# Kernel optimization log

Measured on AMD Instinct MI355X. Metric: run time of the kernel, lower is better.

## Reference

```python
import jax, jax.numpy as jnp
import numpy as np

INPUT_DIM = 2048
N_TREES = 15
TREE_DEPTH = 3
N_LEAVES = 2 ** TREE_DEPTH          # 8
N_INTERNAL = 2 ** TREE_DEPTH - 1    # 7
PARAM_PER_TREE = N_INTERNAL * (INPUT_DIM + 1) + N_LEAVES * 2  # 14375
BATCH = 32768


def setup_inputs() -> dict:
    key = jax.random.key(0)
    k1, k2, k3 = jax.random.split(key, 3)
    x = jax.random.normal(k1, (BATCH, INPUT_DIM), dtype=jnp.float32)
    tree_params = jax.random.normal(k2, (1, N_TREES * PARAM_PER_TREE), dtype=jnp.float32)
    tree_weights = jax.random.uniform(k3, (1, N_TREES), dtype=jnp.float32)
    return {"x": x, "tree_params": tree_params, "tree_weights": tree_weights}


def reference(x, tree_params, tree_weights):
    D, T, I, L = INPUT_DIM, N_TREES, N_INTERNAL, N_LEAVES
    B = x.shape[0]
    p = tree_params[0].reshape(T, PARAM_PER_TREE)
    split_w = p[:, : I * D].reshape(T, I, D)                       # [T, I, D]
    split_b = p[:, I * D : I * (D + 1)]                            # [T, I]
    leaf_logits = p[:, I * (D + 1) :].reshape(T, L, 2)             # [T, L, 2]

    # One fused GEMM over all trees/nodes: [B, T, I]
    decisions = jax.nn.sigmoid(jnp.einsum('bd,tid->bti', x, split_w) + split_b)

    # Faithful replication of the original gating loop (leaf 0 ungated,
    # internal nodes with child index >= L are no-ops).
    leaf_probs = jnp.ones((B, T, L), dtype=x.dtype)
    for i in range(I):
        left, right = 2 * i + 1, 2 * i + 2
        d = decisions[:, :, i]
        if left < L:
            leaf_probs = leaf_probs.at[:, :, left].multiply(d)
        if right < L:
            leaf_probs = leaf_probs.at[:, :, right].multiply(1.0 - d)

    leaf_probs = leaf_probs / (leaf_probs.sum(axis=-1, keepdims=True) + 1e-8)
    leaf_dist = jax.nn.softmax(leaf_logits, axis=-1)               # [T, L, 2]
    tree_out = jnp.einsum('btl,tlc->btc', leaf_probs, leaf_dist)   # [B, T, 2]
    final_probs = jnp.einsum('btc,t->bc', tree_out, tree_weights[0])
    return final_probs
```

## Files before the change

kernel.cpp:

```cpp
#include <hip/hip_runtime.h>
#include <stdint.h>

#define D_IN    2048
#define NT      15
#define PPT     14359
#define NVALID  60

typedef __bf16   bf16x8 __attribute__((ext_vector_type(8)));
typedef float    f32x4  __attribute__((ext_vector_type(4)));
typedef uint32_t u32x4  __attribute__((ext_vector_type(4)));

#define WAITV8 asm volatile("s_waitcnt vmcnt(8)" ::: "memory")
#define WAITV0 asm volatile("s_waitcnt vmcnt(0)" ::: "memory")
#define WAITL0 asm volatile("s_waitcnt lgkmcnt(0)" ::: "memory")
#define SCHEDB __builtin_amdgcn_sched_barrier(0)

__device__ __forceinline__ f32x4 gload4(const float* p) {
  f32x4 r;
  asm volatile("global_load_dwordx4 %0, %1, off" : "=v"(r) : "v"(p) : "memory");
  return r;
}
__device__ __forceinline__ u32x4 dsread16(uint32_t addr) {
  u32x4 r;
  asm volatile("ds_read_b128 %0, %1" : "=v"(r) : "v"(addr) : "memory");
  return r;
}
__device__ __forceinline__ void dswrite16(uint32_t addr, u32x4 v) {
  asm volatile("ds_write_b128 %0, %1" :: "v"(addr), "v"(v) : "memory");
}

#define CVT_PAIR(P, Q, HW, LW) do {                                   \
    uint32_t _up = __float_as_uint(P), _uq = __float_as_uint(Q);      \
    uint32_t _mp = _up & 0xFFFF0000u, _mq = _uq & 0xFFFF0000u;        \
    (HW) = (_up >> 16) | _mq;                                         \
    float _lp = (P) - __uint_as_float(_mp);                           \
    float _lq = (Q) - __uint_as_float(_mq);                           \
    (LW) = (__float_as_uint(_lp) >> 16) |                             \
           (__float_as_uint(_lq) & 0xFFFF0000u);                      \
  } while (0)

__device__ __forceinline__ void cvt8(const f32x4 A, const f32x4 B,
                                     u32x4& hi, u32x4& lo) {
  CVT_PAIR(A[0], A[1], hi[0], lo[0]);
  CVT_PAIR(A[2], A[3], hi[1], lo[1]);
  CVT_PAIR(B[0], B[1], hi[2], lo[2]);
  CVT_PAIR(B[2], B[3], hi[3], lo[3]);
}

#define ITERATION(tt, BUF, WBUF, RC, WA, WB, ISSUE, ENDSTAGE, ENDV0)           \
  {                                                                            \
    __builtin_amdgcn_s_barrier();                                              \
    const uint32_t bb = sbase + (BUF) * 16384 + l16;                           \
    u32x4 bfr[16];                                                             \
    _Pragma("unroll")                                                          \
    for (int q = 0; q < 16; ++q) bfr[q] = dsread16(bb + q * 1024);             \
    u32x4 ah0, al0, ah1, al1;                                                  \
    cvt8(RC[0], RC[1], ah0, al0);                                              \
    cvt8(RC[2], RC[3], ah1, al1);                                              \
    WAITL0; SCHEDB;                                                            \
    if (ISSUE) {                                                               \
      const int t2 = (tt) + 2;                                                 \
      WA[0] = gload4(wp0 + t2 * 64);  WA[1] = gload4(wp0 + t2 * 64 + 4);       \
      WA[2] = gload4(wp1 + t2 * 64);  WA[3] = gload4(wp1 + t2 * 64 + 4);       \
      const float* ap = xbase + t2 * 64;                                       \
      RC[0] = gload4(ap);      RC[1] = gload4(ap + 4);                         \
      RC[2] = gload4(ap + 32); RC[3] = gload4(ap + 36);                        \
    }                                                                          \
    _Pragma("unroll")                                                          \
    for (int f = 0; f < 4; ++f) {                                              \
      bf16x8 bh = __builtin_bit_cast(bf16x8, bfr[f * 2]);                      \
      bf16x8 bl = __builtin_bit_cast(bf16x8, bfr[f * 2 + 1]);                  \
      bf16x8 Ah = __builtin_bit_cast(bf16x8, ah0);                             \
      bf16x8 Al = __builtin_bit_cast(bf16x8, al0);                             \
      acc[f] = __builtin_amdgcn_mfma_f32_16x16x32_bf16(Ah, bh, acc[f], 0,0,0); \
      acc[f] = __builtin_amdgcn_mfma_f32_16x16x32_bf16(Al, bh, acc[f], 0,0,0); \
      acc[f] = __builtin_amdgcn_mfma_f32_16x16x32_bf16(Ah, bl, acc[f], 0,0,0); \
    }                                                                          \
    _Pragma("unroll")                                                          \
    for (int f = 0; f < 4; ++f) {                                              \
      bf16x8 bh = __builtin_bit_cast(bf16x8, bfr[8 + f * 2]);                  \
      bf16x8 bl = __builtin_bit_cast(bf16x8, bfr[8 + f * 2 + 1]);              \
      bf16x8 Ah = __builtin_bit_cast(bf16x8, ah1);                             \
      bf16x8 Al = __builtin_bit_cast(bf16x8, al1);                             \
      acc[f] = __builtin_amdgcn_mfma_f32_16x16x32_bf16(Ah, bh, acc[f], 0,0,0); \
      acc[f] = __builtin_amdgcn_mfma_f32_16x16x32_bf16(Al, bh, acc[f], 0,0,0); \
      acc[f] = __builtin_amdgcn_mfma_f32_16x16x32_bf16(Ah, bl, acc[f], 0,0,0); \
    }                                                                          \
    if (ENDSTAGE) {                                                            \
      if (ENDV0) { WAITV0; } else { WAITV8; }                                  \
      SCHEDB;                                                                  \
      f32x4 w2 = WB[2] * vmask, w3 = WB[3] * vmask;                            \
      u32x4 h0, l0, h1, l1;                                                    \
      cvt8(WB[0], WB[1], h0, l0);                                              \
      cvt8(w2, w3, h1, l1);                                                    \
      const uint32_t wb_ = sbase + (WBUF) * 16384 + w4096 + l16;               \
      dswrite16(wb_,        h0);  dswrite16(wb_ + 1024, l0);                   \
      dswrite16(wb_ + 2048, h1);  dswrite16(wb_ + 3072, l1);                   \
      WAITL0; SCHEDB;                                                          \
    }                                                                          \
  }

__global__ __launch_bounds__(256) void tree_fused(
    const float* __restrict__ x,
    const float* __restrict__ tp,
    const float* __restrict__ tw,
    float* __restrict__ out)
{
  __shared__ __align__(1024) unsigned char sB[3 * 16384];
  __shared__ float strips[4][16][65];
  __shared__ float sBias[64];
  __shared__ float sCoef[160];

  const int tid = threadIdx.x;
  const int w   = tid >> 6;
  const int l   = tid & 63;
  const int rl  = l & 15;
  const int g   = l >> 4;
  const int l16 = l * 16;
  const int w4096 = w * 4096;

  if (tid < 64) {
    float b = 0.0f;
    if (tid < NVALID) { int t = tid >> 2, i = tid & 3; b = tp[t * PPT + 14336 + i]; }
    sBias[tid] = b;
  } else if (tid < 64 + NT) {
    int t = tid - 64;
    const float* ll = tp + t * PPT + 14343;
    float d0[8], d1[8];
#pragma unroll
    for (int le = 0; le < 8; ++le) {
      float aa = ll[2 * le], bb = ll[2 * le + 1];
      float m = fmaxf(aa, bb);
      float e0 = __expf(aa - m), e1 = __expf(bb - m);
      float inv = 1.0f / (e0 + e1);
      d0[le] = e0 * inv; d1[le] = e1 * inv;
    }
    float ww = tw[t];
    float* c = sCoef + t * 10;
    c[0] = ww * (d0[0] + d0[2] + d0[4] + d0[6]);
    c[1] = ww * (d1[0] + d1[2] + d1[4] + d1[6]);
    c[2] = ww * (d0[1] - d0[2]);
    c[3] = ww * (d1[1] - d1[2]);
    c[4] = ww * (d0[3] - d0[4]);
    c[5] = ww * (d1[3] - d1[4]);
    c[6] = ww * (d0[5] - d0[6]);
    c[7] = ww * (d1[5] - d1[6]);
    c[8] = ww * d0[7];
    c[9] = ww * d1[7];
  }
  __syncthreads();

  const int h  = w >> 1;
  const int f0 = 2 * (w & 1);
  const int n0 = 16 * f0 + rl;
  const int n1 = n0 + 16;
  const float vmask = (n1 < NVALID) ? 1.0f : 0.0f;
  const int coloff = h * 32 + g * 8;
  const float* wp0 = tp + (size_t)(n0 >> 2) * PPT + (n0 & 3) * D_IN + coloff;
  const float* wp1r = tp + (size_t)(n1 >> 2) * PPT + (n1 & 3) * D_IN + coloff;
  const float* wp1 = (n1 < NVALID) ? wp1r : tp;

  const int rowTile = blockIdx.x * 64 + w * 16;
  const float* xbase = x + (size_t)(rowTile + rl) * D_IN + g * 8;
  const uint32_t sbase = (uint32_t)(uintptr_t)&sB[0];

  f32x4 acc[4] = {};
  f32x4 rA[4], rB[4];
  f32x4 wWa[4], wWb[4];

  {
    wWa[0] = gload4(wp0);      wWa[1] = gload4(wp0 + 4);
    wWa[2] = gload4(wp1);      wWa[3] = gload4(wp1 + 4);
    rA[0] = gload4(xbase);      rA[1] = gload4(xbase + 4);
    rA[2] = gload4(xbase + 32); rA[3] = gload4(xbase + 36);
    wWb[0] = gload4(wp0 + 64);  wWb[1] = gload4(wp0 + 68);
    wWb[2] = gload4(wp1 + 64);  wWb[3] = gload4(wp1 + 68);
    rB[0] = gload4(xbase + 64); rB[1] = gload4(xbase + 68);
    rB[2] = gload4(xbase + 96); rB[3] = gload4(xbase + 100);
    WAITV8; SCHEDB;
    f32x4 w2 = wWa[2] * vmask, w3 = wWa[3] * vmask;
    u32x4 h0, l0, h1, l1;
    cvt8(wWa[0], wWa[1], h0, l0);
    cvt8(w2, w3, h1, l1);
    const uint32_t wb_ = sbase + w4096 + l16;
    dswrite16(wb_,        h0);  dswrite16(wb_ + 1024, l0);
    dswrite16(wb_ + 2048, h1);  dswrite16(wb_ + 3072, l1);
    WAITL0; SCHEDB;
  }

  for (int tb = 0; tb < 30; tb += 6) {
    ITERATION(tb + 0, 0, 1, rA, wWa, wWb, 1, 1, 0);
    ITERATION(tb + 1, 1, 2, rB, wWb, wWa, 1, 1, 0);
    ITERATION(tb + 2, 2, 0, rA, wWa, wWb, 1, 1, 0);
    ITERATION(tb + 3, 0, 1, rB, wWb, wWa, 1, 1, 0);
    ITERATION(tb + 4, 1, 2, rA, wWa, wWb, 1, 1, 0);
    ITERATION(tb + 5, 2, 0, rB, wWb, wWa, 1, 1, 0);
  }
  ITERATION(30, 0, 1, rA, wWa, wWb, 0, 1, 1);
  ITERATION(31, 1, 2, rB, wWb, wWa, 0, 0, 0);

#pragma unroll
  for (int f = 0; f < 4; ++f)
#pragma unroll
    for (int r = 0; r < 4; ++r)
      strips[w][4 * g + r][16 * f + rl] = acc[f][r];
  WAITL0;

  float o0 = 0.0f, o1 = 0.0f;
#pragma unroll
  for (int jt = 0; jt < 4; ++jt) {
    int t = g + 4 * jt;
    if (t < NT) {
      const float* cf = sCoef + t * 10;
      float dd[4];
#pragma unroll
      for (int i = 0; i < 4; ++i) {
        float z = strips[w][rl][4 * t + i] + sBias[4 * t + i];
        dd[i] = 1.0f / (1.0f + __expf(-z));
      }
      float s = 1.0f / (4.0f + dd[3] + 1e-8f);
      o0 += s * (cf[0] + dd[0] * cf[2] + dd[1] * cf[4] + dd[2] * cf[6] + dd[3] * cf[8]);
      o1 += s * (cf[1] + dd[0] * cf[3] + dd[1] * cf[5] + dd[2] * cf[7] + dd[3] * cf[9]);
    }
  }
  o0 += __shfl_xor(o0, 16); o0 += __shfl_xor(o0, 32);
  o1 += __shfl_xor(o1, 16); o1 += __shfl_xor(o1, 32);
  if (l < 16) {
    ((float2*)out)[rowTile + rl] = make_float2(o0, o1);
  }
}

extern "C" void kernel_launch(void* const* d_in, const int* in_sizes, int n_in,
                              void* d_out, int out_size, void* d_ws, size_t ws_size,
                              hipStream_t stream) {
  (void)in_sizes; (void)n_in; (void)out_size; (void)d_ws; (void)ws_size;
  const float* x  = (const float*)d_in[0];
  const float* tp = (const float*)d_in[1];
  const float* tw = (const float*)d_in[2];
  float* out = (float*)d_out;

  tree_fused<<<512, 256, 0, stream>>>(x, tp, tw, out);
}
```

Measured before the change: 66.94 us.

## Pre-split weights into bf16 hi/lo layout and stream via direct-to-LDS loads

A new prep kernel converts the split weights once into a pre-swizzled bf16 hi/lo buffer in workspace and computes bias and leaf coefficients there. The main kernel then copies weight tiles straight into LDS with global_load_lds, deepens the pipeline to four LDS buffers (prefetch distance three), and drops the per-block conversion and ds_write work. This removes redundant weight conversion across all 512 blocks, in exchange for an extra kernel launch, more LDS per block, and reuse of sB for the output strips.

```diff
diff --git a/kernel.cpp b/kernel.cpp
--- a/kernel.cpp
+++ b/kernel.cpp
@@ -10,24 +10,9 @@
 typedef float    f32x4  __attribute__((ext_vector_type(4)));
 typedef uint32_t u32x4  __attribute__((ext_vector_type(4)));
 
-#define WAITV8 asm volatile("s_waitcnt vmcnt(8)" ::: "memory")
-#define WAITV0 asm volatile("s_waitcnt vmcnt(0)" ::: "memory")
-#define WAITL0 asm volatile("s_waitcnt lgkmcnt(0)" ::: "memory")
-#define SCHEDB __builtin_amdgcn_sched_barrier(0)
-
-__device__ __forceinline__ f32x4 gload4(const float* p) {
-  f32x4 r;
-  asm volatile("global_load_dwordx4 %0, %1, off" : "=v"(r) : "v"(p) : "memory");
-  return r;
-}
-__device__ __forceinline__ u32x4 dsread16(uint32_t addr) {
-  u32x4 r;
-  asm volatile("ds_read_b128 %0, %1" : "=v"(r) : "v"(addr) : "memory");
-  return r;
-}
-__device__ __forceinline__ void dswrite16(uint32_t addr, u32x4 v) {
-  asm volatile("ds_write_b128 %0, %1" :: "v"(addr), "v"(v) : "memory");
-}
+#define WAITV(n) asm volatile("s_waitcnt vmcnt(" #n ")" ::: "memory")
+#define WAITL0   asm volatile("s_waitcnt lgkmcnt(0)" ::: "memory")
+#define SCHEDB   __builtin_amdgcn_sched_barrier(0)
 
 #define CVT_PAIR(P, Q, HW, LW) do {                                   \
     uint32_t _up = __float_as_uint(P), _uq = __float_as_uint(Q);      \
@@ -47,8 +32,83 @@
   CVT_PAIR(B[2], B[3], hi[3], lo[3]);
 }
 
-#define ITERATION(tt, BUF, WBUF, RC, WA, WB, ISSUE, ENDSTAGE, ENDV0)           \
+__global__ __launch_bounds__(256) void prep_split(const float* __restrict__ tp,
+                                                  const float* __restrict__ tw,
+                                                  unsigned short* __restrict__ bsp,
+                                                  float* __restrict__ bias,
+                                                  float* __restrict__ coef) {
+  const int n  = blockIdx.x;
+  const int j  = threadIdx.x;
+  const int k0 = j * 8;
+  f32x4 v0 = {0,0,0,0}, v1 = {0,0,0,0};
+  if (n < NVALID) {
+    const float* src = tp + (size_t)(n >> 2) * PPT + (n & 3) * D_IN + k0;
+#pragma unroll
+    for (int q = 0; q < 4; ++q) v0[q] = src[q];
+#pragma unroll
+    for (int q = 0; q < 4; ++q) v1[q] = src[4 + q];
+  }
+  u32x4 hi, lo;
+  cvt8(v0, v1, hi, lo);
+  const int ks = k0 >> 5, f = n >> 4;
+  const int lane = (n & 15) | (((k0 >> 3) & 3) << 4);
+  char* bb = (char*)bsp + ((size_t)(ks * 4 + f) * 2) * 1024 + (size_t)lane * 16;
+  *(u32x4*)(bb)        = hi;
+  *(u32x4*)(bb + 1024) = lo;
+
+  if (blockIdx.x == 0) {
+    int tid = threadIdx.x;
+    if (tid < 64) {
+      float b = 0.0f;
+      if (tid < NVALID) { int t = tid >> 2, i = tid & 3; b = tp[t * PPT + 14336 + i]; }
+      bias[tid] = b;
+    } else if (tid < 64 + NT) {
+      int t = tid - 64;
+      const float* ll = tp + t * PPT + 14343;
+      float d0[8], d1[8];
+#pragma unroll
+      for (int le = 0; le < 8; ++le) {
+        float aa = ll[2 * le], bb2 = ll[2 * le + 1];
+        float m = fmaxf(aa, bb2);
+        float e0 = __expf(aa - m), e1 = __expf(bb2 - m);
+        float inv = 1.0f / (e0 + e1);
+        d0[le] = e0 * inv; d1[le] = e1 * inv;
+      }
+      float ww = tw[t];
+      float* c = coef + t * 10;
+      c[0] = ww * (d0[0] + d0[2] + d0[4] + d0[6]);
+      c[1] = ww * (d1[0] + d1[2] + d1[4] + d1[6]);
+      c[2] = ww * (d0[1] - d0[2]);
+      c[3] = ww * (d1[1] - d1[2]);
+      c[4] = ww * (d0[3] - d0[4]);
+      c[5] = ww * (d1[3] - d1[4]);
+      c[6] = ww * (d0[5] - d0[6]);
+      c[7] = ww * (d1[5] - d1[6]);
+      c[8] = ww * d0[7];
+      c[9] = ww * d1[7];
+    }
+  }
+}
+
+__device__ __forceinline__ f32x4 gload4(const float* p) {
+  f32x4 r;
+  asm volatile("global_load_dwordx4 %0, %1, off" : "=v"(r) : "v"(p) : "memory");
+  return r;
+}
+__device__ __forceinline__ u32x4 dsread16(uint32_t addr) {
+  u32x4 r;
+  asm volatile("ds_read_b128 %0, %1" : "=v"(r) : "v"(addr) : "memory");
+  return r;
+}
+__device__ __forceinline__ void stage16(const void* g, void* l) {
+  __builtin_amdgcn_global_load_lds(
+      (const __attribute__((address_space(1))) void*)g,
+      (__attribute__((address_space(3))) void*)l, 16, 0, 0);
+}
+
+#define ITERATION(tt, BUF, RC, WN, ISSUE)                                      \
   {                                                                            \
+    WAITV(WN); SCHEDB;                                                         \
     __builtin_amdgcn_s_barrier();                                              \
     const uint32_t bb = sbase + (BUF) * 16384 + l16;                           \
     u32x4 bfr[16];                                                             \
@@ -59,10 +119,12 @@
     cvt8(RC[2], RC[3], ah1, al1);                                              \
     WAITL0; SCHEDB;                                                            \
     if (ISSUE) {                                                               \
-      const int t2 = (tt) + 2;                                                 \
-      WA[0] = gload4(wp0 + t2 * 64);  WA[1] = gload4(wp0 + t2 * 64 + 4);       \
-      WA[2] = gload4(wp1 + t2 * 64);  WA[3] = gload4(wp1 + t2 * 64 + 4);       \
-      const float* ap = xbase + t2 * 64;                                       \
+      const int t3 = (tt) + 3;                                                 \
+      const char* gsrc = bspb + (size_t)t3 * 16384 + w4096l16;                 \
+      char* ldst = sBgen + (((BUF) + 3) & 3) * 16384 + w4096;                  \
+      _Pragma("unroll")                                                        \
+      for (int q = 0; q < 4; ++q) stage16(gsrc + q * 1024, ldst + q * 1024);   \
+      const float* ap = xbase + t3 * 64;                                       \
       RC[0] = gload4(ap);      RC[1] = gload4(ap + 4);                         \
       RC[2] = gload4(ap + 32); RC[3] = gload4(ap + 36);                        \
     }                                                                          \
@@ -86,30 +148,16 @@
       acc[f] = __builtin_amdgcn_mfma_f32_16x16x32_bf16(Al, bh, acc[f], 0,0,0); \
       acc[f] = __builtin_amdgcn_mfma_f32_16x16x32_bf16(Ah, bl, acc[f], 0,0,0); \
     }                                                                          \
-    if (ENDSTAGE) {                                                            \
-      if (ENDV0) { WAITV0; } else { WAITV8; }                                  \
-      SCHEDB;                                                                  \
-      f32x4 w2 = WB[2] * vmask, w3 = WB[3] * vmask;                            \
-      u32x4 h0, l0, h1, l1;                                                    \
-      cvt8(WB[0], WB[1], h0, l0);                                              \
-      cvt8(w2, w3, h1, l1);                                                    \
-      const uint32_t wb_ = sbase + (WBUF) * 16384 + w4096 + l16;               \
-      dswrite16(wb_,        h0);  dswrite16(wb_ + 1024, l0);                   \
-      dswrite16(wb_ + 2048, h1);  dswrite16(wb_ + 3072, l1);                   \
-      WAITL0; SCHEDB;                                                          \
-    }                                                                          \
   }
 
 __global__ __launch_bounds__(256) void tree_fused(
     const float* __restrict__ x,
-    const float* __restrict__ tp,
-    const float* __restrict__ tw,
+    const unsigned short* __restrict__ bsp,
+    const float* __restrict__ bias,
+    const float* __restrict__ coef,
     float* __restrict__ out)
 {
-  __shared__ __align__(1024) unsigned char sB[3 * 16384];
-  __shared__ float strips[4][16][65];
-  __shared__ float sBias[64];
-  __shared__ float sCoef[160];
+  __shared__ __align__(1024) unsigned char sB[4 * 16384];
 
   const int tid = threadIdx.x;
   const int w   = tid >> 6;
@@ -118,87 +166,55 @@
   const int g   = l >> 4;
   const int l16 = l * 16;
   const int w4096 = w * 4096;
-
-  if (tid < 64) {
-    float b = 0.0f;
-    if (tid < NVALID) { int t = tid >> 2, i = tid & 3; b = tp[t * PPT + 14336 + i]; }
-    sBias[tid] = b;
-  } else if (tid < 64 + NT) {
-    int t = tid - 64;
-    const float* ll = tp + t * PPT + 14343;
-    float d0[8], d1[8];
-#pragma unroll
-    for (int le = 0; le < 8; ++le) {
-      float aa = ll[2 * le], bb = ll[2 * le + 1];
-      float m = fmaxf(aa, bb);
-      float e0 = __expf(aa - m), e1 = __expf(bb - m);
-      float inv = 1.0f / (e0 + e1);
-      d0[le] = e0 * inv; d1[le] = e1 * inv;
-    }
-    float ww = tw[t];
-    float* c = sCoef + t * 10;
-    c[0] = ww * (d0[0] + d0[2] + d0[4] + d0[6]);
-    c[1] = ww * (d1[0] + d1[2] + d1[4] + d1[6]);
-    c[2] = ww * (d0[1] - d0[2]);
-    c[3] = ww * (d1[1] - d1[2]);
-    c[4] = ww * (d0[3] - d0[4]);
-    c[5] = ww * (d1[3] - d1[4]);
-    c[6] = ww * (d0[5] - d0[6]);
-    c[7] = ww * (d1[5] - d1[6]);
-    c[8] = ww * d0[7];
-    c[9] = ww * d1[7];
-  }
-  __syncthreads();
-
-  const int h  = w >> 1;
-  const int f0 = 2 * (w & 1);
-  const int n0 = 16 * f0 + rl;
-  const int n1 = n0 + 16;
-  const float vmask = (n1 < NVALID) ? 1.0f : 0.0f;
-  const int coloff = h * 32 + g * 8;
-  const float* wp0 = tp + (size_t)(n0 >> 2) * PPT + (n0 & 3) * D_IN + coloff;
-  const float* wp1r = tp + (size_t)(n1 >> 2) * PPT + (n1 & 3) * D_IN + coloff;
-  const float* wp1 = (n1 < NVALID) ? wp1r : tp;
+  const int w4096l16 = w4096 + l16;
 
   const int rowTile = blockIdx.x * 64 + w * 16;
   const float* xbase = x + (size_t)(rowTile + rl) * D_IN + g * 8;
-  const uint32_t sbase = (uint32_t)(uintptr_t)&sB[0];
+  const char* bspb = (const char*)bsp;
+  char* sBgen = (char*)&sB[0];
+  const uint32_t sbase = (uint32_t)(uintptr_t)sBgen;
 
   f32x4 acc[4] = {};
-  f32x4 rA[4], rB[4];
-  f32x4 wWa[4], wWb[4];
+  f32x4 r0[4], r1[4], r2[4];
 
   {
-    wWa[0] = gload4(wp0);      wWa[1] = gload4(wp0 + 4);
-    wWa[2] = gload4(wp1);      wWa[3] = gload4(wp1 + 4);
-    rA[0] = gload4(xbase);      rA[1] = gload4(xbase + 4);
-    rA[2] = gload4(xbase + 32); rA[3] = gload4(xbase + 36);
-    wWb[0] = gload4(wp0 + 64);  wWb[1] = gload4(wp0 + 68);
-    wWb[2] = gload4(wp1 + 64);  wWb[3] = gload4(wp1 + 68);
-    rB[0] = gload4(xbase + 64); rB[1] = gload4(xbase + 68);
-    rB[2] = gload4(xbase + 96); rB[3] = gload4(xbase + 100);
-    WAITV8; SCHEDB;
-    f32x4 w2 = wWa[2] * vmask, w3 = wWa[3] * vmask;
-    u32x4 h0, l0, h1, l1;
-    cvt8(wWa[0], wWa[1], h0, l0);
-    cvt8(w2, w3, h1, l1);
-    const uint32_t wb_ = sbase + w4096 + l16;
-    dswrite16(wb_,        h0);  dswrite16(wb_ + 1024, l0);
-    dswrite16(wb_ + 2048, h1);  dswrite16(wb_ + 3072, l1);
-    WAITL0; SCHEDB;
-  }
-
-  for (int tb = 0; tb < 30; tb += 6) {
-    ITERATION(tb + 0, 0, 1, rA, wWa, wWb, 1, 1, 0);
-    ITERATION(tb + 1, 1, 2, rB, wWb, wWa, 1, 1, 0);
-    ITERATION(tb + 2, 2, 0, rA, wWa, wWb, 1, 1, 0);
-    ITERATION(tb + 3, 0, 1, rB, wWb, wWa, 1, 1, 0);
-    ITERATION(tb + 4, 1, 2, rA, wWa, wWb, 1, 1, 0);
-    ITERATION(tb + 5, 2, 0, rB, wWb, wWa, 1, 1, 0);
-  }
-  ITERATION(30, 0, 1, rA, wWa, wWb, 0, 1, 1);
-  ITERATION(31, 1, 2, rB, wWb, wWa, 0, 0, 0);
-
+#pragma unroll
+    for (int s = 0; s < 3; ++s) {
+      const char* gs = bspb + (size_t)s * 16384 + w4096l16;
+      char* ld = sBgen + s * 16384 + w4096;
+#pragma unroll
+      for (int q = 0; q < 4; ++q) stage16(gs + q * 1024, ld + q * 1024);
+      const float* ap = xbase + s * 64;
+      f32x4* rr = (s == 0) ? r0 : (s == 1) ? r1 : r2;
+      rr[0] = gload4(ap);      rr[1] = gload4(ap + 4);
+      rr[2] = gload4(ap + 32); rr[3] = gload4(ap + 36);
+    }
+  }
+
+  for (int tb = 0; tb < 24; tb += 12) {
+    ITERATION(tb + 0,  0, r0, 16, 1);
+    ITERATION(tb + 1,  1, r1, 16, 1);
+    ITERATION(tb + 2,  2, r2, 16, 1);
+    ITERATION(tb + 3,  3, r0, 16, 1);
+    ITERATION(tb + 4,  0, r1, 16, 1);
+    ITERATION(tb + 5,  1, r2, 16, 1);
+    ITERATION(tb + 6,  2, r0, 16, 1);
+    ITERATION(tb + 7,  3, r1, 16, 1);
+    ITERATION(tb + 8,  0, r2, 16, 1);
+    ITERATION(tb + 9,  1, r0, 16, 1);
+    ITERATION(tb + 10, 2, r1, 16, 1);
+    ITERATION(tb + 11, 3, r2, 16, 1);
+  }
+  ITERATION(24, 0, r0, 16, 1);
+  ITERATION(25, 1, r1, 16, 1);
+  ITERATION(26, 2, r2, 16, 1);
+  ITERATION(27, 3, r0, 16, 1);
+  ITERATION(28, 0, r1, 16, 1);
+  ITERATION(29, 1, r2, 16, 0);
+  ITERATION(30, 2, r0,  8, 0);
+  ITERATION(31, 3, r1,  0, 0);
+
+  float (*strips)[16][65] = (float (*)[16][65])sBgen;
 #pragma unroll
   for (int f = 0; f < 4; ++f)
 #pragma unroll
@@ -211,11 +227,11 @@
   for (int jt = 0; jt < 4; ++jt) {
     int t = g + 4 * jt;
     if (t < NT) {
-      const float* cf = sCoef + t * 10;
+      const float* cf = coef + t * 10;
       float dd[4];
 #pragma unroll
       for (int i = 0; i < 4; ++i) {
-        float z = strips[w][rl][4 * t + i] + sBias[4 * t + i];
+        float z = strips[w][rl][4 * t + i] + bias[4 * t + i];
         dd[i] = 1.0f / (1.0f + __expf(-z));
       }
       float s = 1.0f / (4.0f + dd[3] + 1e-8f);
@@ -233,11 +249,16 @@
 extern "C" void kernel_launch(void* const* d_in, const int* in_sizes, int n_in,
                               void* d_out, int out_size, void* d_ws, size_t ws_size,
                               hipStream_t stream) {
-  (void)in_sizes; (void)n_in; (void)out_size; (void)d_ws; (void)ws_size;
+  (void)in_sizes; (void)n_in; (void)out_size; (void)ws_size;
   const float* x  = (const float*)d_in[0];
   const float* tp = (const float*)d_in[1];
   const float* tw = (const float*)d_in[2];
   float* out = (float*)d_out;
 
-  tree_fused<<<512, 256, 0, stream>>>(x, tp, tw, out);
-}
+  unsigned short* bsp = (unsigned short*)d_ws;
+  float* bias = (float*)((char*)d_ws + 524288);
+  float* coef = (float*)((char*)d_ws + 524288 + 256);
+
+  prep_split<<<64, 256, 0, stream>>>(tp, tw, bsp, bias, coef);
+  tree_fused<<<512, 256, 0, stream>>>(x, bsp, bias, coef, out);
+}
```

Measured after the change: 57.33 us, median of 2. 1.17x faster.

## Deepen global prefetch to three stages and move LDS weight writes before MFMAs

Applied to the files above, without the earlier changes.

Extends the register prefetch pipeline from two to three K-tiles in flight, using triple register buffers for x and weights, so global loads are issued three iterations ahead. The LDS store of the next weight tile now happens right after the LDS reads, before the MFMA block, instead of in a separate end stage with its own vmcnt and lgkmcnt waits. Weight column mapping per wave is also reorganised to use cp0/cp1 slots with per-column validity masks. This adds register pressure, which may lower occupancy, in exchange for more latency hiding.

```diff
diff --git a/kernel.cpp b/kernel.cpp
--- a/kernel.cpp
+++ b/kernel.cpp
@@ -10,24 +10,9 @@
 typedef float    f32x4  __attribute__((ext_vector_type(4)));
 typedef uint32_t u32x4  __attribute__((ext_vector_type(4)));
 
-#define WAITV8 asm volatile("s_waitcnt vmcnt(8)" ::: "memory")
-#define WAITV0 asm volatile("s_waitcnt vmcnt(0)" ::: "memory")
-#define WAITL0 asm volatile("s_waitcnt lgkmcnt(0)" ::: "memory")
-#define SCHEDB __builtin_amdgcn_sched_barrier(0)
-
-__device__ __forceinline__ f32x4 gload4(const float* p) {
-  f32x4 r;
-  asm volatile("global_load_dwordx4 %0, %1, off" : "=v"(r) : "v"(p) : "memory");
-  return r;
-}
-__device__ __forceinline__ u32x4 dsread16(uint32_t addr) {
-  u32x4 r;
-  asm volatile("ds_read_b128 %0, %1" : "=v"(r) : "v"(addr) : "memory");
-  return r;
-}
-__device__ __forceinline__ void dswrite16(uint32_t addr, u32x4 v) {
-  asm volatile("ds_write_b128 %0, %1" :: "v"(addr), "v"(v) : "memory");
-}
+#define WAITV(n) asm volatile("s_waitcnt vmcnt(" #n ")" ::: "memory")
+#define WAITL0   asm volatile("s_waitcnt lgkmcnt(0)" ::: "memory")
+#define SCHEDB   __builtin_amdgcn_sched_barrier(0)
 
 #define CVT_PAIR(P, Q, HW, LW) do {                                   \
     uint32_t _up = __float_as_uint(P), _uq = __float_as_uint(Q);      \
@@ -47,22 +32,49 @@
   CVT_PAIR(B[2], B[3], hi[3], lo[3]);
 }
 
-#define ITERATION(tt, BUF, WBUF, RC, WA, WB, ISSUE, ENDSTAGE, ENDV0)           \
+__device__ __forceinline__ f32x4 gload4(const float* p) {
+  f32x4 r;
+  asm volatile("global_load_dwordx4 %0, %1, off" : "=v"(r) : "v"(p) : "memory");
+  return r;
+}
+__device__ __forceinline__ u32x4 dsread16(uint32_t addr) {
+  u32x4 r;
+  asm volatile("ds_read_b128 %0, %1" : "=v"(r) : "v"(addr) : "memory");
+  return r;
+}
+__device__ __forceinline__ void dswrite16(uint32_t addr, u32x4 v) {
+  asm volatile("ds_write_b128 %0, %1" :: "v"(addr), "v"(v) : "memory");
+}
+
+#define ITERATION(tt, BUF, WBUF, WCON, WISS, RC, WN, ISSUE, DOWRITE)           \
   {                                                                            \
+    WAITV(WN); SCHEDB;                                                         \
     __builtin_amdgcn_s_barrier();                                              \
     const uint32_t bb = sbase + (BUF) * 16384 + l16;                           \
     u32x4 bfr[16];                                                             \
     _Pragma("unroll")                                                          \
     for (int q = 0; q < 16; ++q) bfr[q] = dsread16(bb + q * 1024);             \
+    if (DOWRITE) {                                                             \
+      f32x4 s0 = WCON[0] * vm0, s1 = WCON[1] * vm0;                            \
+      f32x4 s2 = WCON[2] * vm1, s3 = WCON[3] * vm1;                            \
+      u32x4 h0, lo0, h1, lo1;                                                  \
+      cvt8(s0, s1, h0, lo0);                                                   \
+      cvt8(s2, s3, h1, lo1);                                                   \
+      const uint32_t wbb = sbase + (WBUF) * 16384 + l16;                       \
+      dswrite16(wbb + cp0 * 2048,        h0);                                  \
+      dswrite16(wbb + cp0 * 2048 + 1024, lo0);                                 \
+      dswrite16(wbb + cp1 * 2048,        h1);                                  \
+      dswrite16(wbb + cp1 * 2048 + 1024, lo1);                                 \
+    }                                                                          \
     u32x4 ah0, al0, ah1, al1;                                                  \
     cvt8(RC[0], RC[1], ah0, al0);                                              \
     cvt8(RC[2], RC[3], ah1, al1);                                              \
     WAITL0; SCHEDB;                                                            \
     if (ISSUE) {                                                               \
-      const int t2 = (tt) + 2;                                                 \
-      WA[0] = gload4(wp0 + t2 * 64);  WA[1] = gload4(wp0 + t2 * 64 + 4);       \
-      WA[2] = gload4(wp1 + t2 * 64);  WA[3] = gload4(wp1 + t2 * 64 + 4);       \
-      const float* ap = xbase + t2 * 64;                                       \
+      const int t3 = (tt) + 3;                                                 \
+      WISS[0] = gload4(wsrc0 + t3 * 64);  WISS[1] = gload4(wsrc0 + t3 * 64 + 4); \
+      WISS[2] = gload4(wsrc1 + t3 * 64);  WISS[3] = gload4(wsrc1 + t3 * 64 + 4); \
+      const float* ap = xbase + t3 * 64;                                       \
       RC[0] = gload4(ap);      RC[1] = gload4(ap + 4);                         \
       RC[2] = gload4(ap + 32); RC[3] = gload4(ap + 36);                        \
     }                                                                          \
@@ -85,18 +97,6 @@
       acc[f] = __builtin_amdgcn_mfma_f32_16x16x32_bf16(Ah, bh, acc[f], 0,0,0); \
       acc[f] = __builtin_amdgcn_mfma_f32_16x16x32_bf16(Al, bh, acc[f], 0,0,0); \
       acc[f] = __builtin_amdgcn_mfma_f32_16x16x32_bf16(Ah, bl, acc[f], 0,0,0); \
-    }                                                                          \
-    if (ENDSTAGE) {                                                            \
-      if (ENDV0) { WAITV0; } else { WAITV8; }                                  \
-      SCHEDB;                                                                  \
-      f32x4 w2 = WB[2] * vmask, w3 = WB[3] * vmask;                            \
-      u32x4 h0, l0, h1, l1;                                                    \
-      cvt8(WB[0], WB[1], h0, l0);                                              \
-      cvt8(w2, w3, h1, l1);                                                    \
-      const uint32_t wb_ = sbase + (WBUF) * 16384 + w4096 + l16;               \
-      dswrite16(wb_,        h0);  dswrite16(wb_ + 1024, l0);                   \
-      dswrite16(wb_ + 2048, h1);  dswrite16(wb_ + 3072, l1);                   \
-      WAITL0; SCHEDB;                                                          \
     }                                                                          \
   }
 
@@ -117,7 +117,6 @@
   const int rl  = l & 15;
   const int g   = l >> 4;
   const int l16 = l * 16;
-  const int w4096 = w * 4096;
 
   if (tid < 64) {
     float b = 0.0f;
@@ -129,9 +128,9 @@
     float d0[8], d1[8];
 #pragma unroll
     for (int le = 0; le < 8; ++le) {
-      float aa = ll[2 * le], bb = ll[2 * le + 1];
-      float m = fmaxf(aa, bb);
-      float e0 = __expf(aa - m), e1 = __expf(bb - m);
+      float aa = ll[2 * le], bb2 = ll[2 * le + 1];
+      float m = fmaxf(aa, bb2);
+      float e0 = __expf(aa - m), e1 = __expf(bb2 - m);
       float inv = 1.0f / (e0 + e1);
       d0[le] = e0 * inv; d1[le] = e1 * inv;
     }
@@ -149,55 +148,68 @@
     c[9] = ww * d1[7];
   }
   __syncthreads();
-
-  const int h  = w >> 1;
-  const int f0 = 2 * (w & 1);
-  const int n0 = 16 * f0 + rl;
-  const int n1 = n0 + 16;
-  const float vmask = (n1 < NVALID) ? 1.0f : 0.0f;
-  const int coloff = h * 32 + g * 8;
-  const float* wp0 = tp + (size_t)(n0 >> 2) * PPT + (n0 & 3) * D_IN + coloff;
-  const float* wp1r = tp + (size_t)(n1 >> 2) * PPT + (n1 & 3) * D_IN + coloff;
-  const float* wp1 = (n1 < NVALID) ? wp1r : tp;
+  WAITV(0);
+  SCHEDB;
+
+  const int c0 = 2 * w,     c1 = 2 * w + 1;
+  const int h0_ = c0 >> 2,  f0_ = c0 & 3;
+  const int h1_ = c1 >> 2,  f1_ = c1 & 3;
+  const int cp0 = h0_ * 4 + f0_;
+  const int cp1 = h1_ * 4 + f1_;
+  const int n0 = 16 * f0_ + rl;
+  const int n1 = 16 * f1_ + rl;
+  const float vm0 = (n0 < NVALID) ? 1.0f : 0.0f;
+  const float vm1 = (n1 < NVALID) ? 1.0f : 0.0f;
+  const float* wsrc0 = tp + (size_t)((n0 < NVALID ? n0 : 0) >> 2) * PPT
+                          + ((n0 < NVALID ? n0 : 0) & 3) * D_IN + 32 * h0_ + 8 * g;
+  const float* wsrc1 = tp + (size_t)((n1 < NVALID ? n1 : 0) >> 2) * PPT
+                          + ((n1 < NVALID ? n1 : 0) & 3) * D_IN + 32 * h1_ + 8 * g;
 
   const int rowTile = blockIdx.x * 64 + w * 16;
   const float* xbase = x + (size_t)(rowTile + rl) * D_IN + g * 8;
   const uint32_t sbase = (uint32_t)(uintptr_t)&sB[0];
 
   f32x4 acc[4] = {};
-  f32x4 rA[4], rB[4];
-  f32x4 wWa[4], wWb[4];
+  f32x4 ra0[4], ra1[4], ra2[4];
+  f32x4 wb0[4], wb1[4], wb2[4];
 
   {
-    wWa[0] = gload4(wp0);      wWa[1] = gload4(wp0 + 4);
-    wWa[2] = gload4(wp1);      wWa[3] = gload4(wp1 + 4);
-    rA[0] = gload4(xbase);      rA[1] = gload4(xbase + 4);
-    rA[2] = gload4(xbase + 32); rA[3] = gload4(xbase + 36);
-    wWb[0] = gload4(wp0 + 64);  wWb[1] = gload4(wp0 + 68);
-    wWb[2] = gload4(wp1 + 64);  wWb[3] = gload4(wp1 + 68);
-    rB[0] = gload4(xbase + 64); rB[1] = gload4(xbase + 68);
-    rB[2] = gload4(xbase + 96); rB[3] = gload4(xbase + 100);
-    WAITV8; SCHEDB;
-    f32x4 w2 = wWa[2] * vmask, w3 = wWa[3] * vmask;
-    u32x4 h0, l0, h1, l1;
-    cvt8(wWa[0], wWa[1], h0, l0);
-    cvt8(w2, w3, h1, l1);
-    const uint32_t wb_ = sbase + w4096 + l16;
-    dswrite16(wb_,        h0);  dswrite16(wb_ + 1024, l0);
-    dswrite16(wb_ + 2048, h1);  dswrite16(wb_ + 3072, l1);
+    wb0[0] = gload4(wsrc0);       wb0[1] = gload4(wsrc0 + 4);
+    wb0[2] = gload4(wsrc1);       wb0[3] = gload4(wsrc1 + 4);
+    ra0[0] = gload4(xbase);       ra0[1] = gload4(xbase + 4);
+    ra0[2] = gload4(xbase + 32);  ra0[3] = gload4(xbase + 36);
+    wb1[0] = gload4(wsrc0 + 64);  wb1[1] = gload4(wsrc0 + 68);
+    wb1[2] = gload4(wsrc1 + 64);  wb1[3] = gload4(wsrc1 + 68);
+    ra1[0] = gload4(xbase + 64);  ra1[1] = gload4(xbase + 68);
+    ra1[2] = gload4(xbase + 96);  ra1[3] = gload4(xbase + 100);
+    wb2[0] = gload4(wsrc0 + 128); wb2[1] = gload4(wsrc0 + 132);
+    wb2[2] = gload4(wsrc1 + 128); wb2[3] = gload4(wsrc1 + 132);
+    ra2[0] = gload4(xbase + 128); ra2[1] = gload4(xbase + 132);
+    ra2[2] = gload4(xbase + 160); ra2[3] = gload4(xbase + 164);
+    WAITV(16); SCHEDB;
+    f32x4 s0 = wb0[0] * vm0, s1 = wb0[1] * vm0;
+    f32x4 s2 = wb0[2] * vm1, s3 = wb0[3] * vm1;
+    u32x4 h0, lo0, h1, lo1;
+    cvt8(s0, s1, h0, lo0);
+    cvt8(s2, s3, h1, lo1);
+    const uint32_t wbb = sbase + l16;
+    dswrite16(wbb + cp0 * 2048,        h0);
+    dswrite16(wbb + cp0 * 2048 + 1024, lo0);
+    dswrite16(wbb + cp1 * 2048,        h1);
+    dswrite16(wbb + cp1 * 2048 + 1024, lo1);
     WAITL0; SCHEDB;
   }
 
-  for (int tb = 0; tb < 30; tb += 6) {
-    ITERATION(tb + 0, 0, 1, rA, wWa, wWb, 1, 1, 0);
-    ITERATION(tb + 1, 1, 2, rB, wWb, wWa, 1, 1, 0);
-    ITERATION(tb + 2, 2, 0, rA, wWa, wWb, 1, 1, 0);
-    ITERATION(tb + 3, 0, 1, rB, wWb, wWa, 1, 1, 0);
-    ITERATION(tb + 4, 1, 2, rA, wWa, wWb, 1, 1, 0);
-    ITERATION(tb + 5, 2, 0, rB, wWb, wWa, 1, 1, 0);
-  }
-  ITERATION(30, 0, 1, rA, wWa, wWb, 0, 1, 1);
-  ITERATION(31, 1, 2, rB, wWb, wWa, 0, 0, 0);
+  for (int tb = 0; tb < 27; tb += 3) {
+    ITERATION(tb + 0, 0, 1, wb1, wb0, ra0, 8, 1, 1);
+    ITERATION(tb + 1, 1, 2, wb2, wb1, ra1, 8, 1, 1);
+    ITERATION(tb + 2, 2, 0, wb0, wb2, ra2, 8, 1, 1);
+  }
+  ITERATION(27, 0, 1, wb1, wb0, ra0, 8, 1, 1);
+  ITERATION(28, 1, 2, wb2, wb1, ra1, 8, 1, 1);
+  ITERATION(29, 2, 0, wb0, wb2, ra2, 8, 0, 1);
+  ITERATION(30, 0, 1, wb1, wb0, ra0, 0, 0, 1);
+  ITERATION(31, 1, 2, wb2, wb1, ra1, 0, 0, 0);
 
 #pragma unroll
   for (int f = 0; f < 4; ++f)
```

Measured after the change: 71.46 us. +6.8%, slower.
